# Kernel optimization log

Measured on AMD Instinct MI355X. Metric: run time of the kernel, lower is better.

Reference implementation:

```python
import jax, jax.numpy as jnp
import numpy as np

N_NODES = 10000
N_EDGES = 320000
N_REL = 460
N_BASES = 30
D = 200


def setup_inputs() -> dict:
    key = jax.random.key(0)
    k = jax.random.split(key, 8)
    x = jax.random.normal(k[0], (N_NODES, D), dtype=jnp.float32)
    edge_index = jax.random.randint(k[1], (2, N_EDGES), 0, N_NODES, dtype=jnp.int32)
    edge_type = jax.random.randint(k[2], (N_EDGES,), 0, N_REL, dtype=jnp.int32)
    # Xavier-uniform-like init scales
    w_bound = float(np.sqrt(6.0 / (D + D)))
    c_bound = float(np.sqrt(6.0 / (N_REL + N_BASES)))
    weight = jax.random.uniform(k[3], (N_BASES, D, D), minval=-w_bound, maxval=w_bound, dtype=jnp.float32)
    coeff = jax.random.uniform(k[4], (N_REL, N_BASES), minval=-c_bound, maxval=c_bound, dtype=jnp.float32)
    self_weight = jax.random.uniform(k[5], (D, D), minval=-w_bound, maxval=w_bound, dtype=jnp.float32)
    bias = jnp.zeros((D,), dtype=jnp.float32)
    return {
        "x": x,
        "weight": weight,
        "coeff": coeff,
        "self_weight": self_weight,
        "bias": bias,
        "edge_index": edge_index,
        "edge_type": edge_type,
        "num_nodes": N_NODES,
    }


def reference(x, weight, coeff, self_weight, bias, edge_index, edge_type, num_nodes):
    # RelationalGraphConv.forward:
    #   W_r = sum_b coeff[r, b] * V_b ; msg_e = x[src_e] @ W_{type_e}
    #   out[n] = (sum_{e: tgt_e = n} msg_e) / max(in_deg[n], 1) + x @ W_self + bias
    src = edge_index[0]
    tgt = edge_index[1]
    src_feats = x[src]                    # (E, d_in) gather
    edge_coeff = coeff[edge_type]         # (E, B) gather

    # msg_e = sum_b coeff[type_e, b] * (src_e @ V_b): scan over bases to avoid
    # materializing an (E, B, d_out) intermediate (same math as W_r = coeff @ V).
    def body(acc, inputs):
        Vb, cb = inputs                   # (d_in, d_out), (E,)
        return acc + (src_feats @ Vb) * cb[:, None], None

    msg0 = jnp.zeros((src.shape[0], weight.shape[2]), dtype=x.dtype)
    msg, _ = jax.lax.scan(body, msg0, (weight, edge_coeff.T))  # (E, d_out)

    out = jax.ops.segment_sum(msg, tgt, num_segments=num_nodes)              # (N, d_out)
    deg = jax.ops.segment_sum(jnp.ones_like(tgt, dtype=x.dtype), tgt, num_segments=num_nodes)
    out = out / jnp.clip(deg, 1.0)[:, None]
    out = out + x @ self_weight + bias
    return out
```

## Files before the change

### kernel.cpp

```cpp
#include <hip/hip_runtime.h>
#include <hip/hip_bf16.h>

#define N_NODES 10000
#define N_EDGES 320000
#define N_REL   460
#define N_BASES 30
#define DIM     200
#define KZ      6016
#define KT      6240
#define NSTEPS  195
#define NTILES  157
#define NFRAG   16
#define KSPLIT  6
#define PROWS   10048
#define TKELEM  2048

using short8  = __attribute__((ext_vector_type(8))) short;
using floatx4 = __attribute__((ext_vector_type(4))) float;

__device__ __forceinline__ unsigned short f2bf(float f) {
    union { float f; unsigned u; } v; v.f = f;
    unsigned u = v.u;
    return (unsigned short)((u + 0x7fffu + ((u >> 16) & 1u)) >> 16);
}

__device__ __forceinline__ short8 pack8(const unsigned short* u) {
    union { unsigned short s[8]; short8 v; } p;
#pragma unroll
    for (int i = 0; i < 8; ++i) p.s[i] = u[i];
    return p.v;
}

__device__ __forceinline__ size_t asw_idx(int n, int c) {
    int t = n >> 6, sub = (n >> 4) & 3, rl = n & 15;
    int kk = c >> 5, w = c & 31;
    return (size_t)(t * NSTEPS + kk) * TKELEM + sub * 512 + rl * 32 + w;
}


__global__ void hist_kernel(const int* tgt, int* deg) {
    int e = blockIdx.x * blockDim.x + threadIdx.x;
    if (e < N_EDGES) atomicAdd(&deg[tgt[e]], 1);
}

__global__ __launch_bounds__(1024) void scan_kernel(const int* deg, int* starts,
                                                    int* cursor, float* dinv) {
    __shared__ int part[1024];
    int tid = threadIdx.x;
    const int PER = (N_NODES + 1023) / 1024;
    int base = tid * PER;
    int s = 0;
    for (int i = 0; i < PER; ++i) { int idx = base + i; if (idx < N_NODES) s += deg[idx]; }
    part[tid] = s; __syncthreads();
    for (int off = 1; off < 1024; off <<= 1) {
        int v = (tid >= off) ? part[tid - off] : 0;
        __syncthreads();
        part[tid] += v;
        __syncthreads();
    }
    int run = (tid > 0) ? part[tid - 1] : 0;
    for (int i = 0; i < PER; ++i) {
        int idx = base + i;
        if (idx < N_NODES) {
            int d = deg[idx];
            starts[idx] = run; cursor[idx] = run;
            dinv[idx] = 1.0f / (float)(d > 0 ? d : 1);
            run += d;
        }
    }
    if (tid == 1023) starts[N_NODES] = part[1023];
}

__global__ void scatter_kernel(const int* src, const int* tgt, const int* etype,
                               int* cursor, int2* sedge) {
    int e = blockIdx.x * blockDim.x + threadIdx.x;
    if (e < N_EDGES) {
        int t = tgt[e];
        int pos = atomicAdd(&cursor[t], 1);
        sedge[pos] = make_int2(src[e], etype[e]);
    }
}


__global__ void fill_b_kernel(const float* weight, const float* sw, unsigned short* BSW) {
    int idx = blockIdx.x * blockDim.x + threadIdx.x;
    if (idx >= NFRAG * NSTEPS * 512) return;
    int f = idx / (NSTEPS * 512);
    int rem = idx - f * (NSTEPS * 512);
    int kk = rem / 512;
    int e = rem - kk * 512;
    int l = e >> 3, j = e & 7;
    int rB = f * 16 + (l & 15);
    int k  = kk * 32 + (l >> 4) * 8 + j;
    float v = 0.f;
    if (rB < DIM) {
        if (k < KZ) {
            if (k < N_BASES * DIM) {
                int b = k / DIM, kc = k - b * DIM;
                v = weight[(b * DIM + kc) * DIM + rB];
            }
        } else {
            int jj = k - KZ;
            if (jj < DIM) v = sw[jj * DIM + rB];
        }
    }
    BSW[idx] = f2bf(v);
}

__global__ void fill_x_kernel(const float* x, const int* deg,
                              unsigned short* Xbf, unsigned short* ASW) {
    int idx = blockIdx.x * blockDim.x + threadIdx.x;
    if (idx >= N_NODES * 224) return;
    int n = idx / 224, j = idx - n * 224;
    float v = (j < DIM) ? x[(size_t)n * DIM + j] : 0.f;
    if (j < DIM) Xbf[(size_t)n * DIM + j] = f2bf(v);
    int d = deg[n]; if (d < 1) d = 1;
    ASW[asw_idx(n, KZ + j)] = f2bf((float)d * v);
}

__global__ void fill_cpair_kernel(const float* coeff, unsigned int* Cpair) {
    int idx = blockIdx.x * blockDim.x + threadIdx.x;
    if (idx >= N_REL * 16) return;
    int t = idx >> 4, m = idx & 15;
    unsigned lo = f2bf(coeff[t * N_BASES + m]);
    unsigned hi = (m + 16 < N_BASES) ? f2bf(coeff[t * N_BASES + m + 16]) : 0u;
    Cpair[idx] = lo | (hi << 16);
}


__global__ __launch_bounds__(256) void agg_kernel(const unsigned short* __restrict__ Xbf,
                                                  const unsigned int* __restrict__ Cpair,
                                                  const int* __restrict__ starts,
                                                  const int2* __restrict__ sedge,
                                                  unsigned short* __restrict__ ASW) {
    __shared__ __align__(16) unsigned short zbuf[4][3232];
    int lane = threadIdx.x & 63;
    int wave = threadIdx.x >> 6;
    int n = blockIdx.x * 4 + wave;
    int ln = lane & 15, q = lane >> 4;

    floatx4 acc0[13], acc1[13];
#pragma unroll
    for (int f = 0; f < 13; ++f) {
        acc0[f] = (floatx4){0.f, 0.f, 0.f, 0.f};
        acc1[f] = acc0[f];
    }

    int e0 = starts[n], e1 = starts[n + 1];
    for (int kb = e0; kb < e1; kb += 32) {
        int eb = kb + 8 * q;
        unsigned short a0v[8], a1v[8];
        int srcs[8];
#pragma unroll
        for (int j = 0; j < 8; ++j) {
            int e = eb + j;
            int ec = (e < e1) ? e : (e1 - 1);
            int2 sd = sedge[ec];
            unsigned cp = (e < e1) ? Cpair[sd.y * 16 + ln] : 0u;
            a0v[j] = (unsigned short)(cp & 0xffffu);
            a1v[j] = (unsigned short)(cp >> 16);
            srcs[j] = sd.x;
        }
        short8 A0 = pack8(a0v), A1 = pack8(a1v);

        unsigned short bv[2][8];
#pragma unroll
        for (int j = 0; j < 8; ++j)
            bv[0][j] = Xbf[(size_t)srcs[j] * DIM + ln];
#pragma unroll
        for (int f = 0; f < 13; ++f) {
            int cur = f & 1, nxt = cur ^ 1;
            if (f < 12) {
#pragma unroll
                for (int j = 0; j < 8; ++j)
                    bv[nxt][j] = Xbf[(size_t)srcs[j] * DIM + (f + 1) * 16 + ln];
            }
            short8 B = pack8(bv[cur]);
            acc0[f] = __builtin_amdgcn_mfma_f32_16x16x32_bf16(A0, B, acc0[f], 0, 0, 0);
            acc1[f] = __builtin_amdgcn_mfma_f32_16x16x32_bf16(A1, B, acc1[f], 0, 0, 0);
        }
    }

    unsigned short* zb = zbuf[wave];
    int t = n >> 6, sub = (n >> 4) & 3, rl = n & 15;
    const uint4* zb4 = (const uint4*)zb;
    uint4* dst = (uint4*)ASW;
    size_t base_u4 = (size_t)t * NSTEPS * 256 + sub * 64 + rl * 4;

#pragma unroll
    for (int f = 0; f < 13; ++f) {
        int d = f * 16 + ln;
        if (d < DIM) {
#pragma unroll
            for (int i = 0; i < 4; ++i)
                zb[(q * 4 + i) * DIM + d] = f2bf(acc0[f][i]);
        }
    }
    for (int v = lane; v < 400; v += 64) {
        int kk = v >> 2, w8 = v & 3;
        dst[base_u4 + (size_t)kk * 256 + w8] = zb4[v];
    }

    if (lane < 16) zb[2800 + lane] = 0;
#pragma unroll
    for (int f = 0; f < 13; ++f) {
        int d = f * 16 + ln;
        if (d < DIM) {
#pragma unroll
            for (int i = 0; i < 4; ++i) {
                int b1 = 16 + q * 4 + i;
                if (b1 < N_BASES) zb[(b1 - 16) * DIM + d] = f2bf(acc1[f][i]);
            }
        }
    }
    for (int v = lane; v < 352; v += 64) {
        int kk = 100 + (v >> 2), w8 = v & 3;
        dst[base_u4 + (size_t)kk * 256 + w8] = zb4[v];
    }
}


__global__ __launch_bounds__(256) void gemm_kernel(const unsigned short* __restrict__ ASW,
                                                   const unsigned short* __restrict__ BSW,
                                                   float* __restrict__ part) {
    int tid = threadIdx.x;
    int lane = tid & 63, wave = tid >> 6;
    int tile = blockIdx.x, chunk = blockIdx.y;
    int ks = (chunk * NSTEPS) / KSPLIT;
    int ke = ((chunk + 1) * NSTEPS) / KSPLIT;
    int ln = lane & 15, q = lane >> 4;

    const unsigned short* pa = ASW + (size_t)tile * NSTEPS * TKELEM + ln * 32 + q * 8;
    const unsigned short* pb = BSW + (size_t)(wave * NSTEPS) * 512 + lane * 8;

    floatx4 acc[4][4];
#pragma unroll
    for (int i = 0; i < 4; ++i)
#pragma unroll
        for (int s = 0; s < 4; ++s) acc[i][s] = (floatx4){0.f, 0.f, 0.f, 0.f};

    short8 a0[4], b0[4], a1[4], b1[4];

    auto lda = [&](short8* dst, int k) {
#pragma unroll
        for (int s = 0; s < 4; ++s)
            dst[s] = *(const short8*)(pa + (size_t)k * TKELEM + s * 512);
    };
    auto ldb = [&](short8* dst, int k) {
#pragma unroll
        for (int i = 0; i < 4; ++i)
            dst[i] = *(const short8*)(pb + ((size_t)i * 4 * NSTEPS + k) * 512);
    };
    auto mfma16 = [&](short8* a, short8* b) {
#pragma unroll
        for (int i = 0; i < 4; ++i)
#pragma unroll
            for (int s = 0; s < 4; ++s)
                acc[i][s] = __builtin_amdgcn_mfma_f32_16x16x32_bf16(a[s], b[i], acc[i][s], 0, 0, 0);
    };

    lda(a0, ks); ldb(b0, ks);
    int k1 = (ks + 1 < ke) ? ks + 1 : ks;
    lda(a1, k1); ldb(b1, k1);

    int kk = ks;
    for (; kk + 2 < ke; kk += 2) {
        mfma16(a0, b0);
        lda(a0, kk + 2); ldb(b0, kk + 2);
        mfma16(a1, b1);
        int k3 = (kk + 3 < ke) ? kk + 3 : ke - 1;
        lda(a1, k3); ldb(b1, k3);
    }
    mfma16(a0, b0);
    if (kk + 1 < ke) mfma16(a1, b1);

    int row0 = tile * 64;
    float* pbase = part + ((size_t)chunk * PROWS + row0) * 208;
#pragma unroll
    for (int i = 0; i < 4; ++i) {
        int fg = wave + 4 * i;
        if (fg < 13) {
            int c = fg * 16 + ln;
#pragma unroll
            for (int s = 0; s < 4; ++s)
#pragma unroll
                for (int ii = 0; ii < 4; ++ii)
                    pbase[(s * 16 + q * 4 + ii) * 208 + c] = acc[i][s][ii];
        }
    }
}


__global__ __launch_bounds__(256) void reduce_kernel(const float* __restrict__ part,
                                                     const float* __restrict__ dinv,
                                                     const float* __restrict__ bias,
                                                     float* __restrict__ out) {
    int idx = blockIdx.x * blockDim.x + threadIdx.x;
    if (idx >= N_NODES * 50) return;
    int r = idx / 50, cq = idx - r * 50;
    float4 s = {0.f, 0.f, 0.f, 0.f};
#pragma unroll
    for (int c = 0; c < KSPLIT; ++c) {
        float4 v = *(const float4*)(part + ((size_t)c * PROWS + r) * 208 + cq * 4);
        s.x += v.x; s.y += v.y; s.z += v.z; s.w += v.w;
    }
    float dv = dinv[r];
    float4 b = *(const float4*)(bias + cq * 4);
    float4 o;
    o.x = s.x * dv + b.x; o.y = s.y * dv + b.y;
    o.z = s.z * dv + b.z; o.w = s.w * dv + b.w;
    *(float4*)(out + (size_t)r * DIM + cq * 4) = o;
}


extern "C" void kernel_launch(void* const* d_in, const int* in_sizes, int n_in,
                              void* d_out, int out_size, void* d_ws, size_t ws_size,
                              hipStream_t stream) {
    const float* x      = (const float*)d_in[0];
    const float* weight = (const float*)d_in[1];
    const float* coeff  = (const float*)d_in[2];
    const float* selfw  = (const float*)d_in[3];
    const float* bias   = (const float*)d_in[4];
    const int*   eidx   = (const int*)d_in[5];
    const int*   etype  = (const int*)d_in[6];
    const int* src = eidx;
    const int* tgt = eidx + N_EDGES;
    float* out = (float*)d_out;

    char* ws = (char*)d_ws;
    size_t off = 0;
    auto carve = [&](size_t bytes) {
        char* p = ws + off;
        off += (bytes + 255) & ~(size_t)255;
        return p;
    };
    unsigned short* ASW  = (unsigned short*)carve((size_t)NTILES * NSTEPS * TKELEM * 2);
    unsigned short* BSW  = (unsigned short*)carve((size_t)NFRAG * NSTEPS * 512 * 2);
    float* part   = (float*)carve((size_t)KSPLIT * PROWS * 208 * 4);
    unsigned short* Xbf  = (unsigned short*)carve((size_t)(N_NODES * DIM + 64) * 2);
    unsigned int*  Cpair = (unsigned int*)carve((size_t)N_REL * 16 * 4);
    int*   deg    = (int*)carve((size_t)N_NODES * 4);
    int*   starts = (int*)carve((size_t)(N_NODES + 1) * 4);
    int*   cursor = (int*)carve((size_t)N_NODES * 4);
    float* dinv   = (float*)carve((size_t)N_NODES * 4);
    int2*  sedge  = (int2*)carve((size_t)N_EDGES * 8);

    hipMemsetAsync(deg, 0, (size_t)N_NODES * 4, stream);
    hist_kernel<<<(N_EDGES + 255) / 256, 256, 0, stream>>>(tgt, deg);
    scan_kernel<<<1, 1024, 0, stream>>>(deg, starts, cursor, dinv);
    scatter_kernel<<<(N_EDGES + 255) / 256, 256, 0, stream>>>(src, tgt, etype, cursor, sedge);

    fill_b_kernel<<<(NFRAG * NSTEPS * 512 + 255) / 256, 256, 0, stream>>>(weight, selfw, BSW);
    fill_x_kernel<<<(N_NODES * 224 + 255) / 256, 256, 0, stream>>>(x, deg, Xbf, ASW);
    fill_cpair_kernel<<<(N_REL * 16 + 255) / 256, 256, 0, stream>>>(coeff, Cpair);

    agg_kernel<<<N_NODES / 4, 256, 0, stream>>>(Xbf, Cpair, starts, sedge, ASW);

    dim3 ggrid(NTILES, KSPLIT);
    gemm_kernel<<<ggrid, 256, 0, stream>>>(ASW, BSW, part);

    reduce_kernel<<<(N_NODES * 50 + 255) / 256, 256, 0, stream>>>(part, dinv, bias, out);
}
```

Before: 261.5 us.

## Store split-K partials in bf16 tile layout and double K split

The GEMM partial sums are now written as bf16 in a per-tile, per-fragment blocked layout instead of fp32 row-major, and the K dimension is split 12 ways instead of 6 to raise the block count. The reduce kernel reads 16 contiguous bf16 values per thread, widens them to fp32, sums across splits and writes the output row segment. This cuts partial-buffer traffic per split while adding more GEMM blocks. The cost is extra rounding error from bf16 partials and less coalesced scalar output stores in the reduce.

```diff
diff --git a/kernel.cpp b/kernel.cpp
--- a/kernel.cpp
+++ b/kernel.cpp
@@ -11,8 +11,7 @@
 #define NSTEPS  195
 #define NTILES  157
 #define NFRAG   16
-#define KSPLIT  6
-#define PROWS   10048
+#define KSPLIT  12
 #define TKELEM  2048
 
 using short8  = __attribute__((ext_vector_type(8))) short;
@@ -22,6 +21,11 @@
     union { float f; unsigned u; } v; v.f = f;
     unsigned u = v.u;
     return (unsigned short)((u + 0x7fffu + ((u >> 16) & 1u)) >> 16);
+}
+
+__device__ __forceinline__ float bf2f(unsigned short b) {
+    union { unsigned u; float f; } v; v.u = (unsigned)b << 16;
+    return v.f;
 }
 
 __device__ __forceinline__ short8 pack8(const unsigned short* u) {
@@ -222,7 +226,7 @@
 
 __global__ __launch_bounds__(256) void gemm_kernel(const unsigned short* __restrict__ ASW,
                                                    const unsigned short* __restrict__ BSW,
-                                                   float* __restrict__ part) {
+                                                   unsigned short* __restrict__ part) {
     int tid = threadIdx.x;
     int lane = tid & 63, wave = tid >> 6;
     int tile = blockIdx.x, chunk = blockIdx.y;
@@ -274,42 +278,56 @@
     mfma16(a0, b0);
     if (kk + 1 < ke) mfma16(a1, b1);
 
-    int row0 = tile * 64;
-    float* pbase = part + ((size_t)chunk * PROWS + row0) * 208;
+    unsigned short* pbase = part + ((size_t)chunk * NTILES + tile) * 13 * 1024;
 #pragma unroll
     for (int i = 0; i < 4; ++i) {
         int fg = wave + 4 * i;
         if (fg < 13) {
-            int c = fg * 16 + ln;
+            unsigned short* pf = pbase + fg * 1024 + ln;
 #pragma unroll
             for (int s = 0; s < 4; ++s)
 #pragma unroll
                 for (int ii = 0; ii < 4; ++ii)
-                    pbase[(s * 16 + q * 4 + ii) * 208 + c] = acc[i][s][ii];
-        }
-    }
-}
-
-
-__global__ __launch_bounds__(256) void reduce_kernel(const float* __restrict__ part,
+                    pf[(s * 16 + q * 4 + ii) * 16] = f2bf(acc[i][s][ii]);
+        }
+    }
+}
+
+
+__global__ __launch_bounds__(256) void reduce_kernel(const unsigned short* __restrict__ part,
                                                      const float* __restrict__ dinv,
                                                      const float* __restrict__ bias,
                                                      float* __restrict__ out) {
     int idx = blockIdx.x * blockDim.x + threadIdx.x;
-    if (idx >= N_NODES * 50) return;
-    int r = idx / 50, cq = idx - r * 50;
-    float4 s = {0.f, 0.f, 0.f, 0.f};
+    if (idx >= NTILES * 13 * 64) return;
+    int tile = idx / (13 * 64);
+    int rem  = idx - tile * (13 * 64);
+    int fg = rem >> 6, row = rem & 63;
+    int n = tile * 64 + row;
+    if (n >= N_NODES) return;
+
+    float s[16];
+#pragma unroll
+    for (int j = 0; j < 16; ++j) s[j] = 0.f;
 #pragma unroll
     for (int c = 0; c < KSPLIT; ++c) {
-        float4 v = *(const float4*)(part + ((size_t)c * PROWS + r) * 208 + cq * 4);
-        s.x += v.x; s.y += v.y; s.z += v.z; s.w += v.w;
-    }
-    float dv = dinv[r];
-    float4 b = *(const float4*)(bias + cq * 4);
-    float4 o;
-    o.x = s.x * dv + b.x; o.y = s.y * dv + b.y;
-    o.z = s.z * dv + b.z; o.w = s.w * dv + b.w;
-    *(float4*)(out + (size_t)r * DIM + cq * 4) = o;
+        const uint4* p = (const uint4*)(part + (((size_t)c * NTILES + tile) * 13 + fg) * 1024 + row * 16);
+        uint4 v0 = p[0], v1 = p[1];
+        unsigned w[8] = {v0.x, v0.y, v0.z, v0.w, v1.x, v1.y, v1.z, v1.w};
+#pragma unroll
+        for (int h = 0; h < 8; ++h) {
+            union { unsigned u; float f; } lo, hi;
+            lo.u = w[h] << 16; hi.u = w[h] & 0xffff0000u;
+            s[2 * h] += lo.f; s[2 * h + 1] += hi.f;
+        }
+    }
+    float dv = dinv[n];
+    int c0 = fg * 16;
+    int lim = (c0 + 16 <= DIM) ? 16 : DIM - c0;
+    float* orow = out + (size_t)n * DIM + c0;
+#pragma unroll
+    for (int j = 0; j < 16; ++j)
+        if (j < lim) orow[j] = s[j] * dv + bias[c0 + j];
 }
 
 
@@ -336,7 +354,7 @@
     };
     unsigned short* ASW  = (unsigned short*)carve((size_t)NTILES * NSTEPS * TKELEM * 2);
     unsigned short* BSW  = (unsigned short*)carve((size_t)NFRAG * NSTEPS * 512 * 2);
-    float* part   = (float*)carve((size_t)KSPLIT * PROWS * 208 * 4);
+    unsigned short* part = (unsigned short*)carve((size_t)KSPLIT * NTILES * 13 * 1024 * 2);
     unsigned short* Xbf  = (unsigned short*)carve((size_t)(N_NODES * DIM + 64) * 2);
     unsigned int*  Cpair = (unsigned int*)carve((size_t)N_REL * 16 * 4);
     int*   deg    = (int*)carve((size_t)N_NODES * 4);
@@ -359,5 +377,5 @@
     dim3 ggrid(NTILES, KSPLIT);
     gemm_kernel<<<ggrid, 256, 0, stream>>>(ASW, BSW, part);
 
-    reduce_kernel<<<(N_NODES * 50 + 255) / 256, 256, 0, stream>>>(part, dinv, bias, out);
-}
+    reduce_kernel<<<(NTILES * 13 * 64 + 255) / 256, 256, 0, stream>>>(part, dinv, bias, out);
+}
```

Result: slower. 271.9 us (+4.0%).

## Replace split-K partial buffer and reduce kernel with atomic accumulation into output

Applied to the files above, without the earlier changes.

The three fill kernels are merged into one prep kernel, which also initialises the output to the bias. The GEMM now scales each split-K partial by the inverse degree and atomically adds it into the output, so the partial buffer and the separate reduce kernel are gone. This removes writing and re-reading about 50 MB of partials and two launches. In exchange there are 6-way float atomic adds per output element, and float summation order becomes nondeterministic.

```diff
diff --git a/kernel.cpp b/kernel.cpp
--- a/kernel.cpp
+++ b/kernel.cpp
@@ -12,8 +12,13 @@
 #define NTILES  157
 #define NFRAG   16
 #define KSPLIT  6
-#define PROWS   10048
 #define TKELEM  2048
+
+#define PREP_B  (NFRAG * NSTEPS * 512)
+#define PREP_X  (N_NODES * 224)
+#define PREP_O  (N_NODES * DIM)
+#define PREP_C  (N_REL * 16)
+#define PREP_TOTAL (PREP_B + PREP_X + PREP_O + PREP_C)
 
 using short8  = __attribute__((ext_vector_type(8))) short;
 using floatx4 = __attribute__((ext_vector_type(4))) float;
@@ -82,49 +87,58 @@
 }
 
 
-__global__ void fill_b_kernel(const float* weight, const float* sw, unsigned short* BSW) {
+__global__ void prep_kernel(const float* __restrict__ weight, const float* __restrict__ sw,
+                            const float* __restrict__ x, const float* __restrict__ coeff,
+                            const float* __restrict__ bias, const int* __restrict__ deg,
+                            unsigned short* __restrict__ BSW, unsigned short* __restrict__ Xbf,
+                            unsigned short* __restrict__ ASW, float* __restrict__ out,
+                            unsigned int* __restrict__ Cpair) {
     int idx = blockIdx.x * blockDim.x + threadIdx.x;
-    if (idx >= NFRAG * NSTEPS * 512) return;
-    int f = idx / (NSTEPS * 512);
-    int rem = idx - f * (NSTEPS * 512);
-    int kk = rem / 512;
-    int e = rem - kk * 512;
-    int l = e >> 3, j = e & 7;
-    int rB = f * 16 + (l & 15);
-    int k  = kk * 32 + (l >> 4) * 8 + j;
-    float v = 0.f;
-    if (rB < DIM) {
-        if (k < KZ) {
-            if (k < N_BASES * DIM) {
-                int b = k / DIM, kc = k - b * DIM;
-                v = weight[(b * DIM + kc) * DIM + rB];
+    if (idx < PREP_B) {
+        int f = idx / (NSTEPS * 512);
+        int rem = idx - f * (NSTEPS * 512);
+        int kk = rem / 512;
+        int e = rem - kk * 512;
+        int l = e >> 3, j = e & 7;
+        int rB = f * 16 + (l & 15);
+        int k  = kk * 32 + (l >> 4) * 8 + j;
+        float v = 0.f;
+        if (rB < DIM) {
+            if (k < KZ) {
+                if (k < N_BASES * DIM) {
+                    int b = k / DIM, kc = k - b * DIM;
+                    v = weight[(b * DIM + kc) * DIM + rB];
+                }
+            } else {
+                int jj = k - KZ;
+                if (jj < DIM) v = sw[jj * DIM + rB];
             }
-        } else {
-            int jj = k - KZ;
-            if (jj < DIM) v = sw[jj * DIM + rB];
-        }
-    }
-    BSW[idx] = f2bf(v);
-}
-
-__global__ void fill_x_kernel(const float* x, const int* deg,
-                              unsigned short* Xbf, unsigned short* ASW) {
-    int idx = blockIdx.x * blockDim.x + threadIdx.x;
-    if (idx >= N_NODES * 224) return;
-    int n = idx / 224, j = idx - n * 224;
-    float v = (j < DIM) ? x[(size_t)n * DIM + j] : 0.f;
-    if (j < DIM) Xbf[(size_t)n * DIM + j] = f2bf(v);
-    int d = deg[n]; if (d < 1) d = 1;
-    ASW[asw_idx(n, KZ + j)] = f2bf((float)d * v);
-}
-
-__global__ void fill_cpair_kernel(const float* coeff, unsigned int* Cpair) {
-    int idx = blockIdx.x * blockDim.x + threadIdx.x;
-    if (idx >= N_REL * 16) return;
-    int t = idx >> 4, m = idx & 15;
-    unsigned lo = f2bf(coeff[t * N_BASES + m]);
-    unsigned hi = (m + 16 < N_BASES) ? f2bf(coeff[t * N_BASES + m + 16]) : 0u;
-    Cpair[idx] = lo | (hi << 16);
+        }
+        BSW[idx] = f2bf(v);
+        return;
+    }
+    idx -= PREP_B;
+    if (idx < PREP_X) {
+        int n = idx / 224, j = idx - n * 224;
+        float v = (j < DIM) ? x[(size_t)n * DIM + j] : 0.f;
+        if (j < DIM) Xbf[(size_t)n * DIM + j] = f2bf(v);
+        int d = deg[n]; if (d < 1) d = 1;
+        ASW[asw_idx(n, KZ + j)] = f2bf((float)d * v);
+        return;
+    }
+    idx -= PREP_X;
+    if (idx < PREP_O) {
+        int c = idx % DIM;
+        out[idx] = bias[c];
+        return;
+    }
+    idx -= PREP_O;
+    if (idx < PREP_C) {
+        int t = idx >> 4, m = idx & 15;
+        unsigned lo = f2bf(coeff[t * N_BASES + m]);
+        unsigned hi = (m + 16 < N_BASES) ? f2bf(coeff[t * N_BASES + m + 16]) : 0u;
+        Cpair[idx] = lo | (hi << 16);
+    }
 }
 
 
@@ -222,7 +236,8 @@
 
 __global__ __launch_bounds__(256) void gemm_kernel(const unsigned short* __restrict__ ASW,
                                                    const unsigned short* __restrict__ BSW,
-                                                   float* __restrict__ part) {
+                                                   const float* __restrict__ dinv,
+                                                   float* __restrict__ out) {
     int tid = threadIdx.x;
     int lane = tid & 63, wave = tid >> 6;
     int tile = blockIdx.x, chunk = blockIdx.y;
@@ -275,41 +290,31 @@
     if (kk + 1 < ke) mfma16(a1, b1);
 
     int row0 = tile * 64;
-    float* pbase = part + ((size_t)chunk * PROWS + row0) * 208;
+    float dv[4][4];
+    int nr[4][4];
+#pragma unroll
+    for (int s = 0; s < 4; ++s)
+#pragma unroll
+        for (int ii = 0; ii < 4; ++ii) {
+            int n = row0 + s * 16 + q * 4 + ii;
+            nr[s][ii] = n;
+            dv[s][ii] = (n < N_NODES) ? dinv[n] : 0.f;
+        }
 #pragma unroll
     for (int i = 0; i < 4; ++i) {
         int fg = wave + 4 * i;
-        if (fg < 13) {
-            int c = fg * 16 + ln;
+        int c = fg * 16 + ln;
+        if (fg < 13 && c < DIM) {
 #pragma unroll
             for (int s = 0; s < 4; ++s)
 #pragma unroll
-                for (int ii = 0; ii < 4; ++ii)
-                    pbase[(s * 16 + q * 4 + ii) * 208 + c] = acc[i][s][ii];
-        }
-    }
-}
-
-
-__global__ __launch_bounds__(256) void reduce_kernel(const float* __restrict__ part,
-                                                     const float* __restrict__ dinv,
-                                                     const float* __restrict__ bias,
-                                                     float* __restrict__ out) {
-    int idx = blockIdx.x * blockDim.x + threadIdx.x;
-    if (idx >= N_NODES * 50) return;
-    int r = idx / 50, cq = idx - r * 50;
-    float4 s = {0.f, 0.f, 0.f, 0.f};
-#pragma unroll
-    for (int c = 0; c < KSPLIT; ++c) {
-        float4 v = *(const float4*)(part + ((size_t)c * PROWS + r) * 208 + cq * 4);
-        s.x += v.x; s.y += v.y; s.z += v.z; s.w += v.w;
-    }
-    float dv = dinv[r];
-    float4 b = *(const float4*)(bias + cq * 4);
-    float4 o;
-    o.x = s.x * dv + b.x; o.y = s.y * dv + b.y;
-    o.z = s.z * dv + b.z; o.w = s.w * dv + b.w;
-    *(float4*)(out + (size_t)r * DIM + cq * 4) = o;
+                for (int ii = 0; ii < 4; ++ii) {
+                    int n = nr[s][ii];
+                    if (n < N_NODES)
+                        atomicAdd(&out[(size_t)n * DIM + c], acc[i][s][ii] * dv[s][ii]);
+                }
+        }
+    }
 }
 
 
@@ -336,7 +341,6 @@
     };
     unsigned short* ASW  = (unsigned short*)carve((size_t)NTILES * NSTEPS * TKELEM * 2);
     unsigned short* BSW  = (unsigned short*)carve((size_t)NFRAG * NSTEPS * 512 * 2);
-    float* part   = (float*)carve((size_t)KSPLIT * PROWS * 208 * 4);
     unsigned short* Xbf  = (unsigned short*)carve((size_t)(N_NODES * DIM + 64) * 2);
     unsigned int*  Cpair = (unsigned int*)carve((size_t)N_REL * 16 * 4);
     int*   deg    = (int*)carve((size_t)N_NODES * 4);
@@ -350,14 +354,11 @@
     scan_kernel<<<1, 1024, 0, stream>>>(deg, starts, cursor, dinv);
     scatter_kernel<<<(N_EDGES + 255) / 256, 256, 0, stream>>>(src, tgt, etype, cursor, sedge);
 
-    fill_b_kernel<<<(NFRAG * NSTEPS * 512 + 255) / 256, 256, 0, stream>>>(weight, selfw, BSW);
-    fill_x_kernel<<<(N_NODES * 224 + 255) / 256, 256, 0, stream>>>(x, deg, Xbf, ASW);
-    fill_cpair_kernel<<<(N_REL * 16 + 255) / 256, 256, 0, stream>>>(coeff, Cpair);
+    prep_kernel<<<(PREP_TOTAL + 255) / 256, 256, 0, stream>>>(
+        weight, selfw, x, coeff, bias, deg, BSW, Xbf, ASW, out, Cpair);
 
     agg_kernel<<<N_NODES / 4, 256, 0, stream>>>(Xbf, Cpair, starts, sedge, ASW);
 
     dim3 ggrid(NTILES, KSPLIT);
-    gemm_kernel<<<ggrid, 256, 0, stream>>>(ASW, BSW, part);
-
-    reduce_kernel<<<(N_NODES * 50 + 255) / 256, 256, 0, stream>>>(part, dinv, bias, out);
-}
+    gemm_kernel<<<ggrid, 256, 0, stream>>>(ASW, BSW, dinv, out);
+}
```

After: 301.5 us. 1.15x slower.
